# Optimization experiments

Hardware: AMD Instinct MI355X
Metric: run time of the kernel (lower is better)

Reference implementation:

```python
import jax, jax.numpy as jnp
import numpy as np
from jax import lax

BETA = 0.5          # module default beta
WD_ITERATION = 50   # module default wd_iteration
ERR_TOL = 0.1       # early-exit threshold in IPOT loop
EPS_FILL = 1e-8     # masked_fill value


def setup_inputs() -> dict:
    key = jax.random.key(0)
    k1, k2 = jax.random.split(key)
    bs, N = 128, 512
    # non-negative cost matrix, bs x N x N
    C = jax.random.uniform(k1, (bs, N, N), dtype=jnp.float32)
    # boolean node mask, bs x N; guarantee at least one valid node per graph
    mask = jax.random.uniform(k2, (bs, N)) < 0.8
    mask = mask.at[:, 0].set(True)
    return {"C": C, "bs": bs, "N_s": N, "N_t": N, "mask": mask}


def _ipot_T(C, mask, beta=BETA, iteration=WD_ITERATION):
    m = mask.astype(jnp.float32)                                   # (bs, N)
    mu = (m / jnp.sum(m, axis=1, keepdims=True))[:, :, None]       # (bs, N, 1)
    mv = mu
    T0 = m[:, :, None] * m[:, None, :]                             # bmm(mask, mask^T)
    A = jnp.exp(-C / beta)
    notmask = ~mask[:, :, None]                                    # (bs, N, 1)

    def step(carry, _):
        T, sigma, done = carry
        Q = A * T
        b = jnp.einsum('bnm,bmk->bnk', Q, sigma)                   # Q @ sigma
        b = jnp.where(notmask, EPS_FILL, b)
        delta = mu / b
        a = jnp.einsum('bnm,bnk->bmk', Q, delta)                   # Q^T @ delta
        a = jnp.where(notmask, EPS_FILL, a)
        sigma_new = mv / a
        T_new = delta * Q * jnp.swapaxes(sigma_new, 1, 2)
        err = jnp.max(jnp.sum(jnp.abs(T_new - T), axis=-1))        # global max, as in torch
        # emulate host-side early exit: once converged, freeze state
        T_out = jnp.where(done, T, T_new)
        sigma_out = jnp.where(done, sigma, sigma_new)
        done_out = done | (err < ERR_TOL)
        return (T_out, sigma_out, done_out), None

    (T, _, _), _ = lax.scan(step, (T0, mu, jnp.array(False)), None, length=iteration)
    return T


def reference(C, bs, N_s, N_t, mask):
    T = _ipot_T(C, mask)
    distance = jnp.sum(T * C, axis=(-2, -1))                       # (bs,)
    return (distance, T, C)
```

## Files before the change

kernel.cpp:

```cpp
#include <hip/hip_runtime.h>

#define INVB  2.0f
#define TOL   0.1f
#define EPS   1e-8f
#define NITER 50
#define NP    4

typedef float f32x4 __attribute__((ext_vector_type(4)));


__device__ __forceinline__ float wsum(float v) {
    #pragma unroll
    for (int o = 1; o < 64; o <<= 1) v += __shfl_xor(v, o, 64);
    return v;
}

__device__ __forceinline__ void group_arrive(unsigned* flagp) {
    __hip_atomic_fetch_add(flagp, 1u, __ATOMIC_RELEASE, __HIP_MEMORY_SCOPE_AGENT);
}
__device__ __forceinline__ void group_wait(unsigned* flagp, unsigned target) {
    long sp = 0;
    while (__hip_atomic_load(flagp, __ATOMIC_RELAXED, __HIP_MEMORY_SCOPE_AGENT)
               < target && sp < (1L << 24)) {
        __builtin_amdgcn_s_sleep(2); ++sp;
    }
    (void)__hip_atomic_load(flagp, __ATOMIC_ACQUIRE, __HIP_MEMORY_SCOPE_AGENT);
}

__global__ void k_zero(unsigned* ctrl, int ctrlwords, int* mode,
                       const unsigned* mraw, int nwords) {
    const int t = threadIdx.x;
    for (int i = t; i < ctrlwords; i += 1024) ctrl[i] = 0u;
    __shared__ int sF, sB;
    if (t == 0) { sF = 0; sB = 0; }
    __syncthreads();
    int f = 0, b = 0;
    for (int i = t; i < nwords; i += 1024) {
        unsigned w = mraw[i];
        if (w == 0x3f800000u) f = 1;
        else if (w > 1u)      b = 1;
    }
    if (f) atomicOr(&sF, 1);
    if (b) atomicOr(&sB, 1);
    __syncthreads();
    if (t == 0) *mode = sF ? 2 : (sB ? 1 : 0);
}

__global__ __launch_bounds__(1024, 8) void k_ipot4(
    const float* __restrict__ C, const void* __restrict__ mraw,
    int bs, int N,
    unsigned* err_u, unsigned* flags, float* dpart, const int* mode_p,
    float* apart, float* outD, float* outT, float* outC)
{
    const int g    = blockIdx.x >> 2;
    const int p    = blockIdx.x & 3;
    const int t    = threadIdx.x;
    const int lane = t & 63;
    const int wv   = t >> 6;
    const int NR   = N >> 2;
    const int r0   = p * NR;
    const int rpw  = NR >> 4;
    const float NEG = -__builtin_inff();
    unsigned* flagp = &flags[g * 16];

    __shared__ __align__(16) float m01[512];
    __shared__ __align__(16) float ls_s[512];
    __shared__ __align__(16) float sig_s[512];
    __shared__ __align__(16) float rs_s[512];
    __shared__ float ld_own[128], ldp_own[128], ldr_own[128];
    __shared__ __align__(16) float ap_ws[16][512];
    __shared__ float red_s[16];
    __shared__ float muv_s, cnt_s, errg_s;
    __shared__ unsigned errbits_s;

    {
        const int mode = *mode_p;
        if (t < N) {
            const int idx = g * N + t;
            bool mv;
            if (mode == 1)      mv = ((const unsigned char*)mraw)[idx] != 0;
            else if (mode == 2) mv = ((const float*)mraw)[idx] != 0.0f;
            else                mv = ((const int*)mraw)[idx] != 0;
            m01[t]  = mv ? 1.f : 0.f;
            ls_s[t] = mv ? 0.f : NEG;
            sig_s[t] = 0.f; rs_s[t] = 0.f;
        }
        __syncthreads();
        if (t < N) {
            float v = wsum(m01[t]);
            if (lane == 0) red_s[wv] = v;
        }
        __syncthreads();
        if (t == 0) {
            float cnt = 0.f;
            for (int i = 0; i < (N >> 6); ++i) cnt += red_s[i];
            cnt_s = cnt;
            muv_s = 1.0f / cnt;
        }
        __syncthreads();
    }
    const float muv = muv_s, cnt = cnt_s;
    unsigned rnd = 0;

    const float* wbase = C + ((size_t)g * N + r0 + wv * rpw) * N + lane * 4;
    const int mb0 = lane * 4, mb1 = 256 + lane * 4;

    {
        float4 ca = *(const float4*)(wbase);
        float4 cb = *(const float4*)(wbase + 256);
        const float4 m40 = *(const float4*)(&m01[mb0]);
        const float4 m41 = *(const float4*)(&m01[mb1]);
        float4 fa0 = {0,0,0,0}, fa1 = {0,0,0,0};
        for (int j = 0; j < rpw; ++j) {
            const int jn = (j + 1 < rpw) ? (j + 1) : j;
            const float4 na = *(const float4*)(wbase + (size_t)jn * N);
            const float4 nb = *(const float4*)(wbase + (size_t)jn * N + 256);
            const int lo = wv * rpw + j;
            const bool valid = m01[r0 + lo] != 0.f;
            float4 bt0, bt1;
            bt0.x = m40.x * __expf(-INVB * ca.x);
            bt0.y = m40.y * __expf(-INVB * ca.y);
            bt0.z = m40.z * __expf(-INVB * ca.z);
            bt0.w = m40.w * __expf(-INVB * ca.w);
            bt1.x = m41.x * __expf(-INVB * cb.x);
            bt1.y = m41.y * __expf(-INVB * cb.y);
            bt1.z = m41.z * __expf(-INVB * cb.z);
            bt1.w = m41.w * __expf(-INVB * cb.w);
            float bacc = bt0.x + bt0.y + bt0.z + bt0.w
                       + bt1.x + bt1.y + bt1.z + bt1.w;
            bacc = wsum(bacc);
            float q, ld1, ldr;
            if (valid) { q = 1.0f / bacc; ld1 = __logf(q); ldr = bacc; }
            else       { q = 0.f;         ld1 = NEG;       ldr = 0.f;  }
            if (lane == 0) {
                ld_own[lo]  = ld1;
                ldp_own[lo] = valid ? 0.f : NEG;
                ldr_own[lo] = ldr;
            }
            fa0.x += q * bt0.x; fa0.y += q * bt0.y;
            fa0.z += q * bt0.z; fa0.w += q * bt0.w;
            fa1.x += q * bt1.x; fa1.y += q * bt1.y;
            fa1.z += q * bt1.z; fa1.w += q * bt1.w;
            ca = na; cb = nb;
        }
        *(float4*)&ap_ws[wv][mb0] = fa0;
        *(float4*)&ap_ws[wv][mb1] = fa1;
    }
    __syncthreads();
    if (t < N) {
        float av = 0.f;
        #pragma unroll
        for (int w = 0; w < 16; ++w) av += ap_ws[w][t];
        apart[((size_t)(g * NP + p)) * N + t] = av;
    }
    __syncthreads();
    ++rnd;
    if (t == 0) { group_arrive(flagp); group_wait(flagp, NP * rnd); }
    __syncthreads();
    if (t < N && m01[t] != 0.f) {
        float av = 0.f;
        #pragma unroll
        for (int q2 = 0; q2 < NP; ++q2)
            av += apart[((size_t)(g * NP + q2)) * N + t];
        const float sg = muv / av;
        ls_s[t] += __logf(sg);
        sig_s[t] = sg;
        rs_s[t]  = av * cnt;
    }
    __syncthreads();

    int kf = NITER;
    for (int it = 0; it < NITER; ++it) {
        const float s1 = (float)it * INVB;
        if (t == 0) errbits_s = 0u;
        __syncthreads();
        {
            float4 ca = *(const float4*)(wbase);
            float4 cb = *(const float4*)(wbase + 256);
            float4 fa0 = {0,0,0,0}, fa1 = {0,0,0,0};
            float errmax = 0.f;
            for (int j = 0; j < rpw; ++j) {
                const int jn = (j + 1 < rpw) ? (j + 1) : j;
                const float4 na = *(const float4*)(wbase + (size_t)jn * N);
                const float4 nb = *(const float4*)(wbase + (size_t)jn * N + 256);
                const int lo = wv * rpw + j;
                const bool valid = m01[r0 + lo] != 0.f;
                const float ldn = ld_own[lo];
                const float ldr = ldr_own[lo];
                const float4 ln0 = *(const float4*)(&ls_s[mb0]);
                const float4 ln1 = *(const float4*)(&ls_s[mb1]);
                const float4 sg0 = *(const float4*)(&sig_s[mb0]);
                const float4 sg1 = *(const float4*)(&sig_s[mb1]);
                const float4 rs0 = *(const float4*)(&rs_s[mb0]);
                const float4 rs1 = *(const float4*)(&rs_s[mb1]);
                float eacc = 0.f, bacc = 0.f;
                float4 bt0, bt1;
                #define IPOT_E(cc, LN, SG, RS, BT)                          \
                  { float F  = __expf(-INVB * (cc));                        \
                    float G  = __expf(ldn + (LN) - s1 * (cc));              \
                    float tn = G * F;                                       \
                    float to = G * ldr * (RS);                              \
                    eacc += fabsf(tn - to);                                 \
                    (BT) = tn * F * (SG);                                   \
                    bacc += (BT); }
                IPOT_E(ca.x, ln0.x, sg0.x, rs0.x, bt0.x)
                IPOT_E(ca.y, ln0.y, sg0.y, rs0.y, bt0.y)
                IPOT_E(ca.z, ln0.z, sg0.z, rs0.z, bt0.z)
                IPOT_E(ca.w, ln0.w, sg0.w, rs0.w, bt0.w)
                IPOT_E(cb.x, ln1.x, sg1.x, rs1.x, bt1.x)
                IPOT_E(cb.y, ln1.y, sg1.y, rs1.y, bt1.y)
                IPOT_E(cb.z, ln1.z, sg1.z, rs1.z, bt1.z)
                IPOT_E(cb.w, ln1.w, sg1.w, rs1.w, bt1.w)
                #undef IPOT_E
                bacc = wsum(bacc);
                eacc = wsum(eacc);
                errmax = fmaxf(errmax, eacc);
                float q, ldn2, ldrn;
                if (valid) { q = muv / bacc; ldn2 = ldn + __logf(q); ldrn = bacc * cnt; }
                else       { q = 0.f;        ldn2 = NEG;             ldrn = 0.f;       }
                if (lane == 0) {
                    ldp_own[lo] = ldn;
                    ld_own[lo]  = ldn2;
                    ldr_own[lo] = ldrn;
                }
                fa0.x += q * bt0.x * rs0.x; fa0.y += q * bt0.y * rs0.y;
                fa0.z += q * bt0.z * rs0.z; fa0.w += q * bt0.w * rs0.w;
                fa1.x += q * bt1.x * rs1.x; fa1.y += q * bt1.y * rs1.y;
                fa1.z += q * bt1.z * rs1.z; fa1.w += q * bt1.w * rs1.w;
                ca = na; cb = nb;
            }
            if (lane == 0) atomicMax(&errbits_s, __float_as_uint(errmax));
            *(float4*)&ap_ws[wv][mb0] = fa0;
            *(float4*)&ap_ws[wv][mb1] = fa1;
        }
        __syncthreads();
        if (t < N) {
            float av = 0.f;
            #pragma unroll
            for (int w = 0; w < 16; ++w) av += ap_ws[w][t];
            apart[((size_t)(g * NP + p)) * N + t] = av;
        }
        if (t == 0) atomicMax(&err_u[g * 64 + it], errbits_s);
        __syncthreads();
        ++rnd;
        if (t == 0) {
            group_arrive(flagp); group_wait(flagp, NP * rnd);
            errg_s = __uint_as_float(err_u[g * 64 + it]);
        }
        __syncthreads();
        if (errg_s < TOL) { kf = it + 1; break; }
        if (it == NITER - 1) { kf = NITER; break; }
        if (t < N && m01[t] != 0.f) {
            float av = 0.f;
            #pragma unroll
            for (int q2 = 0; q2 < NP; ++q2)
                av += apart[((size_t)(g * NP + q2)) * N + t];
            const float sg = muv / av;
            ls_s[t] += __logf(sg);
            sig_s[t] = sg;
            rs_s[t]  = av * cnt;
        }
        __syncthreads();
    }

    float dacc = 0.f;
    {
        const float sF = (float)kf * INVB;
        float4 ca = *(const float4*)(wbase);
        float4 cb = *(const float4*)(wbase + 256);
        for (int j = 0; j < rpw; ++j) {
            const int jn = (j + 1 < rpw) ? (j + 1) : j;
            const float4 na = *(const float4*)(wbase + (size_t)jn * N);
            const float4 nb = *(const float4*)(wbase + (size_t)jn * N + 256);
            const int lo = wv * rpw + j;
            const int gr = g * N + r0 + lo;
            const float ldv = ldp_own[lo];
            const float4 ln0 = *(const float4*)(&ls_s[mb0]);
            const float4 ln1 = *(const float4*)(&ls_s[mb1]);
            f32x4 t0, t1;
            t0.x = __expf(ldv + ln0.x - sF * ca.x);
            t0.y = __expf(ldv + ln0.y - sF * ca.y);
            t0.z = __expf(ldv + ln0.z - sF * ca.z);
            t0.w = __expf(ldv + ln0.w - sF * ca.w);
            t1.x = __expf(ldv + ln1.x - sF * cb.x);
            t1.y = __expf(ldv + ln1.y - sF * cb.y);
            t1.z = __expf(ldv + ln1.z - sF * cb.z);
            t1.w = __expf(ldv + ln1.w - sF * cb.w);
            dacc += t0.x * ca.x + t0.y * ca.y + t0.z * ca.z + t0.w * ca.w;
            dacc += t1.x * cb.x + t1.y * cb.y + t1.z * cb.z + t1.w * cb.w;
            f32x4 c0 = { ca.x, ca.y, ca.z, ca.w };
            f32x4 c1 = { cb.x, cb.y, cb.z, cb.w };
            __builtin_nontemporal_store(t0, (f32x4*)(outT + (size_t)gr * N + mb0));
            __builtin_nontemporal_store(t1, (f32x4*)(outT + (size_t)gr * N + mb1));
            __builtin_nontemporal_store(c0, (f32x4*)(outC + (size_t)gr * N + mb0));
            __builtin_nontemporal_store(c1, (f32x4*)(outC + (size_t)gr * N + mb1));
            ca = na; cb = nb;
        }
    }
    dacc = wsum(dacc);
    if (lane == 0) red_s[wv] = dacc;
    __syncthreads();
    ++rnd;
    if (t == 0) {
        float d = 0.f;
        #pragma unroll
        for (int w = 0; w < 16; ++w) d += red_s[w];
        dpart[g * NP + p] = d;
        group_arrive(flagp);
        if (p == 0) {
            group_wait(flagp, NP * rnd);
            float dt = 0.f;
            #pragma unroll
            for (int q2 = 0; q2 < NP; ++q2) dt += dpart[g * NP + q2];
            outD[g] = dt;
        }
    }
}

extern "C" void kernel_launch(void* const* d_in, const int* in_sizes, int n_in,
                              void* d_out, int out_size, void* d_ws, size_t ws_size,
                              hipStream_t stream) {
    const float* C    = (const float*)d_in[0];
    const void*  mask = d_in[4];
    const int R  = in_sizes[4];
    const int N  = in_sizes[0] / R;
    const int bs = R / N;

    unsigned* wsu   = (unsigned*)d_ws;
    unsigned* err_u = wsu;
    unsigned* flags = wsu + (size_t)bs * 64;
    float*    dpart = (float*)(flags + (size_t)bs * 16);
    int*      mode  = (int*)(dpart + (size_t)bs * NP);
    const int ctrlwords = bs * 64 + bs * 16 + bs * NP + 1;
    float*    apart = (float*)(wsu + ((ctrlwords + 255) & ~255));

    float* outD = (float*)d_out;
    float* outT = outD + bs;
    float* outC = outT + (size_t)bs * N * N;

    k_zero<<<1, 1024, 0, stream>>>(wsu, ctrlwords, mode,
                                   (const unsigned*)mask, R / 4);
    k_ipot4<<<bs * NP, 1024, 0, stream>>>(C, mask, bs, N,
                                          err_u, flags, dpart, mode,
                                          apart, outD, outT, outC);
}
```

Measured before the change: 258.3 us.

## Fuse final T/distance epilogue into iteration loop and write C during init pass

```diff
diff --git a/kernel.cpp b/kernel.cpp
--- a/kernel.cpp
+++ b/kernel.cpp
@@ -5,8 +5,6 @@
 #define EPS   1e-8f
 #define NITER 50
 #define NP    4
-
-typedef float f32x4 __attribute__((ext_vector_type(4)));
 
 
 __device__ __forceinline__ float wsum(float v) {
@@ -67,9 +65,10 @@
     __shared__ __align__(16) float ls_s[512];
     __shared__ __align__(16) float sig_s[512];
     __shared__ __align__(16) float rs_s[512];
-    __shared__ float ld_own[128], ldp_own[128], ldr_own[128];
+    __shared__ float ld_own[128], ldr_own[128];
     __shared__ __align__(16) float ap_ws[16][512];
     __shared__ float red_s[16];
+    __shared__ float dred_s[16];
     __shared__ float muv_s, cnt_s, errg_s;
     __shared__ unsigned errbits_s;
 
@@ -108,11 +107,13 @@
     {
         float4 ca = *(const float4*)(wbase);
         float4 cb = *(const float4*)(wbase + 256);
+        float4 da = *(const float4*)(wbase + (size_t)N);
+        float4 db = *(const float4*)(wbase + (size_t)N + 256);
         const float4 m40 = *(const float4*)(&m01[mb0]);
         const float4 m41 = *(const float4*)(&m01[mb1]);
         float4 fa0 = {0,0,0,0}, fa1 = {0,0,0,0};
         for (int j = 0; j < rpw; ++j) {
-            const int jn = (j + 1 < rpw) ? (j + 1) : j;
+            const int jn = (j + 2 < rpw) ? (j + 2) : (rpw - 1);
             const float4 na = *(const float4*)(wbase + (size_t)jn * N);
             const float4 nb = *(const float4*)(wbase + (size_t)jn * N + 256);
             const int lo = wv * rpw + j;
@@ -132,16 +133,15 @@
             float q, ld1, ldr;
             if (valid) { q = 1.0f / bacc; ld1 = __logf(q); ldr = bacc; }
             else       { q = 0.f;         ld1 = NEG;       ldr = 0.f;  }
-            if (lane == 0) {
-                ld_own[lo]  = ld1;
-                ldp_own[lo] = valid ? 0.f : NEG;
-                ldr_own[lo] = ldr;
-            }
+            if (lane == 0) { ld_own[lo] = ld1; ldr_own[lo] = ldr; }
             fa0.x += q * bt0.x; fa0.y += q * bt0.y;
             fa0.z += q * bt0.z; fa0.w += q * bt0.w;
             fa1.x += q * bt1.x; fa1.y += q * bt1.y;
             fa1.z += q * bt1.z; fa1.w += q * bt1.w;
-            ca = na; cb = nb;
+            const size_t grN = ((size_t)(g * N + r0 + lo)) * N;
+            *(float4*)(outC + grN + mb0) = ca;
+            *(float4*)(outC + grN + mb1) = cb;
+            ca = da; cb = db; da = na; db = nb;
         }
         *(float4*)&ap_ws[wv][mb0] = fa0;
         *(float4*)&ap_ws[wv][mb1] = fa1;
@@ -169,7 +169,6 @@
     }
     __syncthreads();
 
-    int kf = NITER;
     for (int it = 0; it < NITER; ++it) {
         const float s1 = (float)it * INVB;
         if (t == 0) errbits_s = 0u;
@@ -177,10 +176,12 @@
         {
             float4 ca = *(const float4*)(wbase);
             float4 cb = *(const float4*)(wbase + 256);
+            float4 da = *(const float4*)(wbase + (size_t)N);
+            float4 db = *(const float4*)(wbase + (size_t)N + 256);
             float4 fa0 = {0,0,0,0}, fa1 = {0,0,0,0};
-            float errmax = 0.f;
+            float errmax = 0.f, dacc = 0.f;
             for (int j = 0; j < rpw; ++j) {
-                const int jn = (j + 1 < rpw) ? (j + 1) : j;
+                const int jn = (j + 2 < rpw) ? (j + 2) : (rpw - 1);
                 const float4 na = *(const float4*)(wbase + (size_t)jn * N);
                 const float4 nb = *(const float4*)(wbase + (size_t)jn * N + 256);
                 const int lo = wv * rpw + j;
@@ -194,23 +195,24 @@
                 const float4 rs0 = *(const float4*)(&rs_s[mb0]);
                 const float4 rs1 = *(const float4*)(&rs_s[mb1]);
                 float eacc = 0.f, bacc = 0.f;
-                float4 bt0, bt1;
-                #define IPOT_E(cc, LN, SG, RS, BT)                          \
+                float4 bt0, bt1, tn0, tn1;
+                #define IPOT_E(cc, LN, SG, RS, BT, TN)                      \
                   { float F  = __expf(-INVB * (cc));                        \
                     float G  = __expf(ldn + (LN) - s1 * (cc));              \
-                    float tn = G * F;                                       \
+                    (TN) = G * F;                                           \
                     float to = G * ldr * (RS);                              \
-                    eacc += fabsf(tn - to);                                 \
-                    (BT) = tn * F * (SG);                                   \
-                    bacc += (BT); }
-                IPOT_E(ca.x, ln0.x, sg0.x, rs0.x, bt0.x)
-                IPOT_E(ca.y, ln0.y, sg0.y, rs0.y, bt0.y)
-                IPOT_E(ca.z, ln0.z, sg0.z, rs0.z, bt0.z)
-                IPOT_E(ca.w, ln0.w, sg0.w, rs0.w, bt0.w)
-                IPOT_E(cb.x, ln1.x, sg1.x, rs1.x, bt1.x)
-                IPOT_E(cb.y, ln1.y, sg1.y, rs1.y, bt1.y)
-                IPOT_E(cb.z, ln1.z, sg1.z, rs1.z, bt1.z)
-                IPOT_E(cb.w, ln1.w, sg1.w, rs1.w, bt1.w)
+                    eacc += fabsf((TN) - to);                               \
+                    (BT) = (TN) * F * (SG);                                 \
+                    bacc += (BT);                                           \
+                    dacc += (TN) * (cc); }
+                IPOT_E(ca.x, ln0.x, sg0.x, rs0.x, bt0.x, tn0.x)
+                IPOT_E(ca.y, ln0.y, sg0.y, rs0.y, bt0.y, tn0.y)
+                IPOT_E(ca.z, ln0.z, sg0.z, rs0.z, bt0.z, tn0.z)
+                IPOT_E(ca.w, ln0.w, sg0.w, rs0.w, bt0.w, tn0.w)
+                IPOT_E(cb.x, ln1.x, sg1.x, rs1.x, bt1.x, tn1.x)
+                IPOT_E(cb.y, ln1.y, sg1.y, rs1.y, bt1.y, tn1.y)
+                IPOT_E(cb.z, ln1.z, sg1.z, rs1.z, bt1.z, tn1.z)
+                IPOT_E(cb.w, ln1.w, sg1.w, rs1.w, bt1.w, tn1.w)
                 #undef IPOT_E
                 bacc = wsum(bacc);
                 eacc = wsum(eacc);
@@ -218,20 +220,21 @@
                 float q, ldn2, ldrn;
                 if (valid) { q = muv / bacc; ldn2 = ldn + __logf(q); ldrn = bacc * cnt; }
                 else       { q = 0.f;        ldn2 = NEG;             ldrn = 0.f;       }
-                if (lane == 0) {
-                    ldp_own[lo] = ldn;
-                    ld_own[lo]  = ldn2;
-                    ldr_own[lo] = ldrn;
-                }
+                if (lane == 0) { ld_own[lo] = ldn2; ldr_own[lo] = ldrn; }
                 fa0.x += q * bt0.x * rs0.x; fa0.y += q * bt0.y * rs0.y;
                 fa0.z += q * bt0.z * rs0.z; fa0.w += q * bt0.w * rs0.w;
                 fa1.x += q * bt1.x * rs1.x; fa1.y += q * bt1.y * rs1.y;
                 fa1.z += q * bt1.z * rs1.z; fa1.w += q * bt1.w * rs1.w;
-                ca = na; cb = nb;
+                const size_t grN = ((size_t)(g * N + r0 + lo)) * N;
+                *(float4*)(outT + grN + mb0) = tn0;
+                *(float4*)(outT + grN + mb1) = tn1;
+                ca = da; cb = db; da = na; db = nb;
             }
             if (lane == 0) atomicMax(&errbits_s, __float_as_uint(errmax));
             *(float4*)&ap_ws[wv][mb0] = fa0;
             *(float4*)&ap_ws[wv][mb1] = fa1;
+            dacc = wsum(dacc);
+            if (lane == 0) dred_s[wv] = dacc;
         }
         __syncthreads();
         if (t < N) {
@@ -240,7 +243,13 @@
             for (int w = 0; w < 16; ++w) av += ap_ws[w][t];
             apart[((size_t)(g * NP + p)) * N + t] = av;
         }
-        if (t == 0) atomicMax(&err_u[g * 64 + it], errbits_s);
+        if (t == 0) {
+            float d = 0.f;
+            #pragma unroll
+            for (int w = 0; w < 16; ++w) d += dred_s[w];
+            dpart[g * NP + p] = d;
+            atomicMax(&err_u[g * 64 + it], errbits_s);
+        }
         __syncthreads();
         ++rnd;
         if (t == 0) {
@@ -248,8 +257,8 @@
             errg_s = __uint_as_float(err_u[g * 64 + it]);
         }
         __syncthreads();
-        if (errg_s < TOL) { kf = it + 1; break; }
-        if (it == NITER - 1) { kf = NITER; break; }
+        if (errg_s < TOL) break;
+        if (it == NITER - 1) break;
         if (t < N && m01[t] != 0.f) {
             float av = 0.f;
             #pragma unroll
@@ -263,57 +272,11 @@
         __syncthreads();
     }
 
-    float dacc = 0.f;
-    {
-        const float sF = (float)kf * INVB;
-        float4 ca = *(const float4*)(wbase);
-        float4 cb = *(const float4*)(wbase + 256);
-        for (int j = 0; j < rpw; ++j) {
-            const int jn = (j + 1 < rpw) ? (j + 1) : j;
-            const float4 na = *(const float4*)(wbase + (size_t)jn * N);
-            const float4 nb = *(const float4*)(wbase + (size_t)jn * N + 256);
-            const int lo = wv * rpw + j;
-            const int gr = g * N + r0 + lo;
-            const float ldv = ldp_own[lo];
-            const float4 ln0 = *(const float4*)(&ls_s[mb0]);
-            const float4 ln1 = *(const float4*)(&ls_s[mb1]);
-            f32x4 t0, t1;
-            t0.x = __expf(ldv + ln0.x - sF * ca.x);
-            t0.y = __expf(ldv + ln0.y - sF * ca.y);
-            t0.z = __expf(ldv + ln0.z - sF * ca.z);
-            t0.w = __expf(ldv + ln0.w - sF * ca.w);
-            t1.x = __expf(ldv + ln1.x - sF * cb.x);
-            t1.y = __expf(ldv + ln1.y - sF * cb.y);
-            t1.z = __expf(ldv + ln1.z - sF * cb.z);
-            t1.w = __expf(ldv + ln1.w - sF * cb.w);
-            dacc += t0.x * ca.x + t0.y * ca.y + t0.z * ca.z + t0.w * ca.w;
-            dacc += t1.x * cb.x + t1.y * cb.y + t1.z * cb.z + t1.w * cb.w;
-            f32x4 c0 = { ca.x, ca.y, ca.z, ca.w };
-            f32x4 c1 = { cb.x, cb.y, cb.z, cb.w };
-            __builtin_nontemporal_store(t0, (f32x4*)(outT + (size_t)gr * N + mb0));
-            __builtin_nontemporal_store(t1, (f32x4*)(outT + (size_t)gr * N + mb1));
-            __builtin_nontemporal_store(c0, (f32x4*)(outC + (size_t)gr * N + mb0));
-            __builtin_nontemporal_store(c1, (f32x4*)(outC + (size_t)gr * N + mb1));
-            ca = na; cb = nb;
-        }
-    }
-    dacc = wsum(dacc);
-    if (lane == 0) red_s[wv] = dacc;
-    __syncthreads();
-    ++rnd;
-    if (t == 0) {
-        float d = 0.f;
+    if (p == 0 && t == 0) {
+        float dt = 0.f;
         #pragma unroll
-        for (int w = 0; w < 16; ++w) d += red_s[w];
-        dpart[g * NP + p] = d;
-        group_arrive(flagp);
-        if (p == 0) {
-            group_wait(flagp, NP * rnd);
-            float dt = 0.f;
-            #pragma unroll
-            for (int q2 = 0; q2 < NP; ++q2) dt += dpart[g * NP + q2];
-            outD[g] = dt;
-        }
+        for (int q2 = 0; q2 < NP; ++q2) dt += dpart[g * NP + q2];
+        outD[g] = dt;
     }
 }
 
```

After: 606.6 us. +134.8%, slower.

## Remap blocks to XCDs, deepen row prefetch, use plain stores for outputs

Applied to the files above, without the earlier changes.

```diff
diff --git a/kernel.cpp b/kernel.cpp
--- a/kernel.cpp
+++ b/kernel.cpp
@@ -5,8 +5,6 @@
 #define EPS   1e-8f
 #define NITER 50
 #define NP    4
-
-typedef float f32x4 __attribute__((ext_vector_type(4)));
 
 
 __device__ __forceinline__ float wsum(float v) {
@@ -52,8 +50,20 @@
     unsigned* err_u, unsigned* flags, float* dpart, const int* mode_p,
     float* apart, float* outD, float* outT, float* outC)
 {
-    const int g    = blockIdx.x >> 2;
-    const int p    = blockIdx.x & 3;
+    int g, p;
+    {
+        const int nblk = bs * NP;
+        const int bid  = blockIdx.x;
+        if ((nblk & (8 * NP - 1)) == 0) {
+            const int xcd = bid & 7;
+            const int slot = bid >> 3;
+            const int gpx = (nblk >> 3) / NP;
+            g = xcd * gpx + (slot >> 2);
+            p = slot & 3;
+        } else {
+            g = bid >> 2; p = bid & 3;
+        }
+    }
     const int t    = threadIdx.x;
     const int lane = t & 63;
     const int wv   = t >> 6;
@@ -108,11 +118,13 @@
     {
         float4 ca = *(const float4*)(wbase);
         float4 cb = *(const float4*)(wbase + 256);
+        float4 da = *(const float4*)(wbase + (size_t)N);
+        float4 db = *(const float4*)(wbase + (size_t)N + 256);
         const float4 m40 = *(const float4*)(&m01[mb0]);
         const float4 m41 = *(const float4*)(&m01[mb1]);
         float4 fa0 = {0,0,0,0}, fa1 = {0,0,0,0};
         for (int j = 0; j < rpw; ++j) {
-            const int jn = (j + 1 < rpw) ? (j + 1) : j;
+            const int jn = (j + 2 < rpw) ? (j + 2) : (rpw - 1);
             const float4 na = *(const float4*)(wbase + (size_t)jn * N);
             const float4 nb = *(const float4*)(wbase + (size_t)jn * N + 256);
             const int lo = wv * rpw + j;
@@ -132,16 +144,12 @@
             float q, ld1, ldr;
             if (valid) { q = 1.0f / bacc; ld1 = __logf(q); ldr = bacc; }
             else       { q = 0.f;         ld1 = NEG;       ldr = 0.f;  }
-            if (lane == 0) {
-                ld_own[lo]  = ld1;
-                ldp_own[lo] = valid ? 0.f : NEG;
-                ldr_own[lo] = ldr;
-            }
+            if (lane == 0) { ld_own[lo] = ld1; ldr_own[lo] = ldr; }
             fa0.x += q * bt0.x; fa0.y += q * bt0.y;
             fa0.z += q * bt0.z; fa0.w += q * bt0.w;
             fa1.x += q * bt1.x; fa1.y += q * bt1.y;
             fa1.z += q * bt1.z; fa1.w += q * bt1.w;
-            ca = na; cb = nb;
+            ca = da; cb = db; da = na; db = nb;
         }
         *(float4*)&ap_ws[wv][mb0] = fa0;
         *(float4*)&ap_ws[wv][mb1] = fa1;
@@ -177,10 +185,12 @@
         {
             float4 ca = *(const float4*)(wbase);
             float4 cb = *(const float4*)(wbase + 256);
+            float4 da = *(const float4*)(wbase + (size_t)N);
+            float4 db = *(const float4*)(wbase + (size_t)N + 256);
             float4 fa0 = {0,0,0,0}, fa1 = {0,0,0,0};
             float errmax = 0.f;
             for (int j = 0; j < rpw; ++j) {
-                const int jn = (j + 1 < rpw) ? (j + 1) : j;
+                const int jn = (j + 2 < rpw) ? (j + 2) : (rpw - 1);
                 const float4 na = *(const float4*)(wbase + (size_t)jn * N);
                 const float4 nb = *(const float4*)(wbase + (size_t)jn * N + 256);
                 const int lo = wv * rpw + j;
@@ -227,7 +237,7 @@
                 fa0.z += q * bt0.z * rs0.z; fa0.w += q * bt0.w * rs0.w;
                 fa1.x += q * bt1.x * rs1.x; fa1.y += q * bt1.y * rs1.y;
                 fa1.z += q * bt1.z * rs1.z; fa1.w += q * bt1.w * rs1.w;
-                ca = na; cb = nb;
+                ca = da; cb = db; da = na; db = nb;
             }
             if (lane == 0) atomicMax(&errbits_s, __float_as_uint(errmax));
             *(float4*)&ap_ws[wv][mb0] = fa0;
@@ -268,8 +278,10 @@
         const float sF = (float)kf * INVB;
         float4 ca = *(const float4*)(wbase);
         float4 cb = *(const float4*)(wbase + 256);
+        float4 da = *(const float4*)(wbase + (size_t)N);
+        float4 db = *(const float4*)(wbase + (size_t)N + 256);
         for (int j = 0; j < rpw; ++j) {
-            const int jn = (j + 1 < rpw) ? (j + 1) : j;
+            const int jn = (j + 2 < rpw) ? (j + 2) : (rpw - 1);
             const float4 na = *(const float4*)(wbase + (size_t)jn * N);
             const float4 nb = *(const float4*)(wbase + (size_t)jn * N + 256);
             const int lo = wv * rpw + j;
@@ -277,7 +289,7 @@
             const float ldv = ldp_own[lo];
             const float4 ln0 = *(const float4*)(&ls_s[mb0]);
             const float4 ln1 = *(const float4*)(&ls_s[mb1]);
-            f32x4 t0, t1;
+            float4 t0, t1;
             t0.x = __expf(ldv + ln0.x - sF * ca.x);
             t0.y = __expf(ldv + ln0.y - sF * ca.y);
             t0.z = __expf(ldv + ln0.z - sF * ca.z);
@@ -288,13 +300,12 @@
             t1.w = __expf(ldv + ln1.w - sF * cb.w);
             dacc += t0.x * ca.x + t0.y * ca.y + t0.z * ca.z + t0.w * ca.w;
             dacc += t1.x * cb.x + t1.y * cb.y + t1.z * cb.z + t1.w * cb.w;
-            f32x4 c0 = { ca.x, ca.y, ca.z, ca.w };
-            f32x4 c1 = { cb.x, cb.y, cb.z, cb.w };
-            __builtin_nontemporal_store(t0, (f32x4*)(outT + (size_t)gr * N + mb0));
-            __builtin_nontemporal_store(t1, (f32x4*)(outT + (size_t)gr * N + mb1));
-            __builtin_nontemporal_store(c0, (f32x4*)(outC + (size_t)gr * N + mb0));
-            __builtin_nontemporal_store(c1, (f32x4*)(outC + (size_t)gr * N + mb1));
-            ca = na; cb = nb;
+            const size_t grN = (size_t)gr * N;
+            *(float4*)(outT + grN + mb0) = t0;
+            *(float4*)(outT + grN + mb1) = t1;
+            *(float4*)(outC + grN + mb0) = ca;
+            *(float4*)(outC + grN + mb1) = cb;
+            ca = da; cb = db; da = na; db = nb;
         }
     }
     dacc = wsum(dacc);
```

New measurement: 339.2 us. +31.3%, slower.
